# Kernel tuning notes

Measured on AMD Instinct MI355X. Metric: run time of the kernel, lower is better.

Reference implementation:

```python
import jax, jax.numpy as jnp
import numpy as np

LOGISTIC_R = 3.8
COUPLING_ITERS = 5


def _linear_interp(v, L):
    """PyTorch F.interpolate(mode='linear', align_corners=False) along last axis.
    v: [..., K] real -> [..., L] real."""
    K = v.shape[-1]
    pos = (jnp.arange(L, dtype=jnp.float32) + 0.5) * (K / L) - 0.5
    pos = jnp.clip(pos, 0.0, K - 1)  # torch clamps src coords into range
    i0 = jnp.floor(pos).astype(jnp.int32)
    i1 = jnp.minimum(i0 + 1, K - 1)
    w = pos - i0
    return v[..., i0] * (1.0 - w) + v[..., i1] * w


def setup_inputs() -> dict:
    key = jax.random.key(0)
    ks = jax.random.split(key, 4)
    B, Cin, Cout, L, K = 16, 64, 64, 8192, 64
    return {
        "x_real": jax.random.normal(ks[0], (B, Cin, L), jnp.float32),
        "x_imag": jax.random.normal(ks[1], (B, Cin, L), jnp.float32),
        "kernel_real": jax.random.normal(ks[2], (Cout, Cin, K), jnp.float32),
        "kernel_imag": jax.random.normal(ks[3], (Cout, Cin, K), jnp.float32),
        "alpha_D": jnp.ones((1,), jnp.float32),
    }


def reference(x_real, x_imag, kernel_real, kernel_imag, alpha_D):
    x = x_real + 1j * x_imag  # [B, Cin, L] complex64
    L = x.shape[-1]

    # --- logistic self-coupling on magnitude (per-batch min/max over (C, L)) ---
    mag = jnp.abs(x)
    phase = jnp.angle(x)
    mmin = mag.min(axis=(-1, -2), keepdims=True)
    mmax = mag.max(axis=(-1, -2), keepdims=True)
    xn = (mag - mmin) / (mmax - mmin + 1e-10)
    for _ in range(COUPLING_ITERS):
        xn = LOGISTIC_R * xn * (1.0 - xn)
    mag_c = xn * (mmax - mmin) + mmin
    x_coupled = mag_c * jnp.exp(1j * phase)

    # --- spectral conv: FFT, per-pair kernel interpolation, complex MAC ---
    x_fft = jnp.fft.fft(x_coupled, axis=-1)  # [B, Cin, L]
    kfft = jnp.fft.fft(kernel_real + 1j * kernel_imag, axis=-1)  # [O, I, K]
    kmag = _linear_interp(jnp.abs(kfft), L)    # [O, I, L]
    kph = _linear_interp(jnp.angle(kfft), L)   # [O, I, L]
    kint = kmag * jnp.exp(1j * kph)            # [O, I, L] complex64
    out_fft = jnp.einsum('bjl,ijl->bil', x_fft, kint)  # replaces O*I python loop
    out = jnp.fft.ifft(out_fft, axis=-1)  # [B, O, L]

    # --- optical probe activation: sin(omega*0 + phi0 + alpha_D * lambda) ---
    theta = alpha_D[0] * jnp.arange(L, dtype=jnp.float32)
    act = jnp.sin(theta)  # omega*t = 0, phi0 = 0
    return out * act
```

## Files before the change

kernel.cpp:

```cpp
#include <hip/hip_runtime.h>
#include <hip/hip_fp16.h>
#include <hip/hip_bf16.h>
#include <math.h>

#define L 8192
#define LOG2L 13
#define B 16
#define CIN 64
#define COUT 64
#define KK 64

#define PI_F 3.14159265358979323846f

typedef float f4v __attribute__((ext_vector_type(4)));
typedef short s8v __attribute__((ext_vector_type(8)));

__device__ __forceinline__ int swz(int n) { return n ^ ((n >> 8) & 31); }
__device__ __forceinline__ int PHI(int n) { return n ^ ((((n >> 5) ^ (n >> 9)) & 15) << 1); }

__device__ __forceinline__ void nsincos(float ang, float* sn, float* cs) {
    float r = ang * 0.15915494309189535f;
    r = r - floorf(r);
    *sn = __builtin_amdgcn_sinf(r);
    *cs = __builtin_amdgcn_cosf(r);
}

__device__ __forceinline__ unsigned short f2bf(float f) {
    unsigned u = __builtin_bit_cast(unsigned, f);
    u += 0x7FFFu + ((u >> 16) & 1u);
    return (unsigned short)(u >> 16);
}
__device__ __forceinline__ unsigned pkbf(float a, float b) {
    unsigned ua = __builtin_bit_cast(unsigned, a) + 0x8000u;
    unsigned ub = __builtin_bit_cast(unsigned, b) + 0x8000u;
    return (ub & 0xFFFF0000u) | (ua >> 16);
}

template<int INV>
__device__ __forceinline__ void bfly4(float& u0r, float& u0i, float& u1r, float& u1i,
                                      float& v0r, float& v0i, float& v1r, float& v1i,
                                      float w1r, float w1i, float w2r, float w2i) {
    float A0r = u0r + v0r, A0i = u0i + v0i;
    float t0r = u0r - v0r, t0i = u0i - v0i;
    float B0r = t0r * w1r - t0i * w1i, B0i = t0r * w1i + t0i * w1r;
    float A1r = u1r + v1r, A1i = u1i + v1i;
    float t1r = u1r - v1r, t1i = u1i - v1i;
    float wr = t1r * w1r - t1i * w1i, wi = t1r * w1i + t1i * w1r;
    float B1r = INV ? -wi : wi;
    float B1i = INV ? wr : -wr;
    u0r = A0r + A1r; u0i = A0i + A1i;
    float d0r = A0r - A1r, d0i = A0i - A1i;
    u1r = d0r * w2r - d0i * w2i; u1i = d0r * w2i + d0i * w2r;
    v0r = B0r + B1r; v0i = B0i + B1i;
    float d1r = B0r - B1r, d1i = B0i - B1i;
    v1r = d1r * w2r - d1i * w2i; v1i = d1r * w2i + d1i * w2r;
}

template<int INV>
__device__ __forceinline__ void radix16(float* xr, float* xi, float wc, float ws) {
    const float C8 = 0.9238795325112867f, S8 = 0.3826834323650898f, C4 = 0.7071067811865476f;
    float e1r = C8, e1i = INV ? S8 : -S8;
    float e2r = C4, e2i = INV ? C4 : -C4;
    float e3r = S8, e3i = INV ? C8 : -C8;
    float a1r[4], a1i[4], a2r[4], a2i[4];
    a1r[0] = wc;                    a1i[0] = ws;
    a1r[1] = wc * e1r - ws * e1i;   a1i[1] = wc * e1i + ws * e1r;
    a1r[2] = wc * e2r - ws * e2i;   a1i[2] = wc * e2i + ws * e2r;
    a1r[3] = wc * e3r - ws * e3i;   a1i[3] = wc * e3i + ws * e3r;
#pragma unroll
    for (int q = 0; q < 4; ++q) {
        a2r[q] = a1r[q] * a1r[q] - a1i[q] * a1i[q];
        a2i[q] = 2.f * a1r[q] * a1i[q];
    }
    float b1r = a2r[0] * a2r[0] - a2i[0] * a2i[0], b1i = 2.f * a2r[0] * a2i[0];
    float b2r = b1r * b1r - b1i * b1i, b2i = 2.f * b1r * b1i;
#pragma unroll
    for (int q = 0; q < 4; ++q)
        bfly4<INV>(xr[q], xi[q], xr[q + 4], xi[q + 4], xr[q + 8], xi[q + 8],
                   xr[q + 12], xi[q + 12], a1r[q], a1i[q], a2r[q], a2i[q]);
#pragma unroll
    for (int c = 0; c < 4; ++c)
        bfly4<INV>(xr[4 * c], xi[4 * c], xr[4 * c + 1], xi[4 * c + 1],
                   xr[4 * c + 2], xi[4 * c + 2], xr[4 * c + 3], xi[4 * c + 3],
                   b1r, b1i, b2r, b2i);
}

__global__ __launch_bounds__(256) void k_reduce1(const float* __restrict__ xr,
                                                 const float* __restrict__ xi,
                                                 float* __restrict__ pmin,
                                                 float* __restrict__ pmax) {
    int bid = blockIdx.x;
    int batch = bid >> 6, slice = bid & 63;
    size_t base = (size_t)batch * CIN * L + (size_t)slice * L;
    int tid = threadIdx.x;
    float mn = 3.4e38f, mx = 0.0f;
    for (int r = 0; r < 32; ++r) {
        int idx = r * 256 + tid;
        float a = xr[base + idx], b = xi[base + idx];
        float m = sqrtf(a * a + b * b);
        mn = fminf(mn, m);
        mx = fmaxf(mx, m);
    }
    __shared__ float smn[4], smx[4];
    for (int off = 32; off >= 1; off >>= 1) {
        mn = fminf(mn, __shfl_down(mn, off));
        mx = fmaxf(mx, __shfl_down(mx, off));
    }
    int wave = tid >> 6;
    if ((tid & 63) == 0) { smn[wave] = mn; smx[wave] = mx; }
    __syncthreads();
    if (tid == 0) {
        for (int w = 1; w < 4; ++w) { mn = fminf(mn, smn[w]); mx = fmaxf(mx, smx[w]); }
        pmin[bid] = mn;
        pmax[bid] = mx;
    }
}

__global__ __launch_bounds__(64) void k_reduce2(const float* __restrict__ pmin,
                                                const float* __restrict__ pmax,
                                                float* __restrict__ mmin,
                                                float* __restrict__ mmax) {
    int b = blockIdx.x, t = threadIdx.x;
    float mn = pmin[b * 64 + t], mx = pmax[b * 64 + t];
    for (int off = 32; off >= 1; off >>= 1) {
        mn = fminf(mn, __shfl_down(mn, off));
        mx = fmaxf(mx, __shfl_down(mx, off));
    }
    if (t == 0) { mmin[b] = mn; mmax[b] = mx; }
}

__global__ __launch_bounds__(64) void k_kstats(const float* __restrict__ kr,
                                               const float* __restrict__ ki,
                                               float* __restrict__ Pmag,
                                               float* __restrict__ Pph) {
    int row = blockIdx.x;
    int k = threadIdx.x;
    __shared__ float sr[64], si[64];
    sr[k] = kr[row * 64 + k];
    si[k] = ki[row * 64 + k];
    __syncthreads();
    float ar = 0.f, ai = 0.f;
    for (int n = 0; n < 64; ++n) {
        int m = (n * k) & 63;
        float ang = -2.0f * PI_F * (float)m * (1.0f / 64.0f);
        float s, c;
        __sincosf(ang, &s, &c);
        ar += sr[n] * c - si[n] * s;
        ai += sr[n] * s + si[n] * c;
    }
    float mag = sqrtf(ar * ar + ai * ai);
    float ph = atan2f(ai, ar);
    int io = row >> 6, jn = row & 63;
    int ic = io >> 4, l15 = io & 15;
    int jc = jn >> 5, hi = (jn >> 3) & 3, e = jn & 7;
    int lane = hi * 16 + l15;
    size_t off = (size_t)k * 4096 + (ic * 2 + jc) * 512 + lane * 8 + e;
    Pmag[off] = mag;
    Pph[off] = ph;
    if (k == 63) {
        Pmag[off + 4096] = mag;
        Pph[off + 4096] = ph;
    }
}

__global__ __launch_bounds__(512) void k_fwd(const float* __restrict__ xr,
                                             const float* __restrict__ xi,
                                             const float* __restrict__ mmin_,
                                             const float* __restrict__ mmax_,
                                             unsigned* __restrict__ xRd) {
    __shared__ float sRe[L];
    __shared__ float sIm[L];
    int row = blockIdx.x;
    int b = row >> 6;
    int tid = threadIdx.x;
    float mmin = mmin_[b], mmax = mmax_[b];
    float span = mmax - mmin;
    float invden = 1.0f / (span + 1e-10f);
    size_t base = (size_t)row * L;

    float vr[16], vi[16];
#pragma unroll
    for (int r = 0; r < 16; ++r) {
        int idx = r * 512 + tid;
        float a = xr[base + idx], c = xi[base + idx];
        float m = sqrtf(a * a + c * c);
        float xn = (m - mmin) * invden;
#pragma unroll
        for (int it = 0; it < 5; ++it) xn = 3.8f * xn * (1.0f - xn);
        float mc = xn * span + mmin;
        float scale = (m > 0.0f) ? (mc / m) : 0.0f;
        vr[r] = a * scale;
        vi[r] = c * scale;
    }
#pragma unroll
    for (int r = 0; r < 8; ++r) {
        float sn, cs;
        nsincos(-PI_F * (float)(r * 512 + tid) * (1.0f / 4096.0f), &sn, &cs);
        float ar = vr[r], ai = vi[r], br = vr[r + 8], bi = vi[r + 8];
        vr[r] = ar + br; vi[r] = ai + bi;
        float dr = ar - br, di = ai - bi;
        vr[r + 8] = dr * cs - di * sn;
        vi[r + 8] = dr * sn + di * cs;
    }
#pragma unroll
    for (int r = 0; r < 16; ++r) {
        int a = PHI(r * 512 + tid);
        sRe[a] = vr[r]; sIm[a] = vi[r];
    }
    __syncthreads();

    {
        int j1 = tid & 255, bA = (tid >> 8) << 12;
#pragma unroll
        for (int m = 0; m < 16; ++m) {
            int a = PHI(bA + j1 + (m << 8));
            vr[m] = sRe[a]; vi[m] = sIm[a];
        }
        float sn, cs;
        nsincos(-PI_F * (float)j1 * (1.0f / 2048.0f), &sn, &cs);
        radix16<0>(vr, vi, cs, sn);
#pragma unroll
        for (int m = 0; m < 16; ++m) {
            int a = PHI(bA + j1 + (m << 8));
            sRe[a] = vr[m]; sIm[a] = vi[m];
        }
    }
    __syncthreads();
    {
        int j1 = tid & 15, bB = (tid >> 4) << 8;
#pragma unroll
        for (int m = 0; m < 16; ++m) {
            int a = PHI(bB + j1 + (m << 4));
            vr[m] = sRe[a]; vi[m] = sIm[a];
        }
        float sn, cs;
        nsincos(-PI_F * (float)j1 * (1.0f / 128.0f), &sn, &cs);
        radix16<0>(vr, vi, cs, sn);
#pragma unroll
        for (int m = 0; m < 16; ++m) {
            int a = PHI(bB + j1 + (m << 4));
            sRe[a] = vr[m]; sIm[a] = vi[m];
        }
    }
    __syncthreads();
    {
        float2* f2R = (float2*)sRe;
        float2* f2I = (float2*)sIm;
#pragma unroll
        for (int m = 0; m < 8; ++m) {
            int a = PHI(tid * 16 + 2 * m) >> 1;
            float2 vR = f2R[a], vI = f2I[a];
            vr[2 * m] = vR.x; vr[2 * m + 1] = vR.y;
            vi[2 * m] = vI.x; vi[2 * m + 1] = vI.y;
        }
        radix16<0>(vr, vi, 1.0f, 0.0f);
#pragma unroll
        for (int m = 0; m < 8; ++m) {
            int a = PHI(tid * 16 + 2 * m) >> 1;
            f2R[a] = make_float2(vr[2 * m], vr[2 * m + 1]);
            f2I[a] = make_float2(vi[2 * m], vi[2 * m + 1]);
        }
    }
    __syncthreads();

#pragma unroll
    for (int r = 0; r < 16; ++r) {
        int a = PHI(r * 512 + tid);
        vr[r] = sRe[a]; vi[r] = sIm[a];
    }
    __syncthreads();
#pragma unroll
    for (int r = 0; r < 16; ++r) {
        int idx = r * 512 + tid;
        int n = (int)(__brev((unsigned)idx) >> 19);
        int a = swz(n);
        sRe[a] = vr[r]; sIm[a] = vi[r];
    }
    __syncthreads();

    unsigned* xId = xRd + (size_t)1024 * 4096;
#pragma unroll
    for (int r = 0; r < 8; ++r) {
        int n2 = r * 1024 + tid * 2;
        int a0 = swz(n2), a1 = swz(n2 + 1);
        unsigned vR = ((unsigned)f2bf(sRe[a1]) << 16) | f2bf(sRe[a0]);
        unsigned vI = ((unsigned)f2bf(sIm[a1]) << 16) | f2bf(sIm[a0]);
        size_t o = (size_t)row * 4096 + (n2 >> 1);
        xRd[o] = vR;
        xId[o] = vI;
    }
}

#define PB 8
#define REG 4624
__global__ __launch_bounds__(256) void k_gemm(const unsigned short* __restrict__ xp,
                                              const float* __restrict__ Pmag,
                                              const float* __restrict__ Pph,
                                              unsigned* __restrict__ outd) {
    __shared__ uint4 ldsbuf[(PB * REG) / 16];
    char* lds = (char*)ldsbuf;
    int tid = threadIdx.x;
    int bid = blockIdx.x;
    int pwin = ((bid & 7) << 7) + (bid >> 3);
    int p0 = pwin * PB;

#pragma unroll
    for (int r = 0; r < 8; ++r) {
        int u = r * 256 + tid;
        int plane = u >> 10;
        int row = u & 1023;
        uint4 v = *(const uint4*)&xp[(size_t)plane * 8388608 + (size_t)row * 8192 + p0];
        int base = plane * 2304 + (row >> 6) * 144 + (row & 63) * 2;
        unsigned short h[8] = {
            (unsigned short)(v.x & 0xFFFF), (unsigned short)(v.x >> 16),
            (unsigned short)(v.y & 0xFFFF), (unsigned short)(v.y >> 16),
            (unsigned short)(v.z & 0xFFFF), (unsigned short)(v.z >> 16),
            (unsigned short)(v.w & 0xFFFF), (unsigned short)(v.w >> 16)};
#pragma unroll
        for (int e = 0; e < 8; ++e)
            *(unsigned short*)&lds[e * REG + base] = h[e];
    }
    __syncthreads();

    int lane = tid & 63;
    int wid = tid >> 6;
    int l15 = lane & 15, l4 = lane >> 4;

    int pA = p0 + wid * 2;
    float posA = ((float)pA + 0.5f) * (1.0f / 128.0f) - 0.5f;
    posA = fmaxf(posA, 0.0f);
    int i0k = (int)posA;
    bool clamp = (i0k >= KK - 1);
    float wq[2];
#pragma unroll
    for (int q = 0; q < 2; ++q) {
        float pos = ((float)(pA + q) + 0.5f) * (1.0f / 128.0f) - 0.5f;
        pos = fmaxf(pos, 0.0f);
        wq[q] = clamp ? 0.0f : (pos - (float)i0k);
    }
    const float* mb0 = Pmag + (size_t)i0k * 4096;
    const float* pb0 = Pph + (size_t)i0k * 4096;

    f4v accR[2][4], accI[2][4];
#pragma unroll
    for (int q = 0; q < 2; ++q)
#pragma unroll
        for (int ic = 0; ic < 4; ++ic) { accR[q][ic] = (f4v)0.0f; accI[q][ic] = (f4v)0.0f; }

#pragma unroll
    for (int jc = 0; jc < 2; ++jc) {
        int jb2 = (jc * 32 + l4 * 8) * 2;
        s8v xR0 = *(const s8v*)&lds[(wid * 2 + 0) * REG + l15 * 144 + jb2];
        s8v xI0 = *(const s8v*)&lds[(wid * 2 + 0) * REG + 2304 + l15 * 144 + jb2];
        s8v xR1 = *(const s8v*)&lds[(wid * 2 + 1) * REG + l15 * 144 + jb2];
        s8v xI1 = *(const s8v*)&lds[(wid * 2 + 1) * REG + 2304 + l15 * 144 + jb2];
#pragma unroll
        for (int ic = 0; ic < 4; ++ic) {
            int tb = (ic * 2 + jc) * 512 + lane * 8;
            float4 m0a = *(const float4*)(mb0 + tb);
            float4 m0b = *(const float4*)(mb0 + tb + 4);
            float4 m1a = *(const float4*)(mb0 + 4096 + tb);
            float4 m1b = *(const float4*)(mb0 + 4096 + tb + 4);
            float4 q0a = *(const float4*)(pb0 + tb);
            float4 q0b = *(const float4*)(pb0 + tb + 4);
            float4 q1a = *(const float4*)(pb0 + 4096 + tb);
            float4 q1b = *(const float4*)(pb0 + 4096 + tb + 4);
            float m0v[8] = {m0a.x, m0a.y, m0a.z, m0a.w, m0b.x, m0b.y, m0b.z, m0b.w};
            float m1v[8] = {m1a.x, m1a.y, m1a.z, m1a.w, m1b.x, m1b.y, m1b.z, m1b.w};
            float q0v[8] = {q0a.x, q0a.y, q0a.z, q0a.w, q0b.x, q0b.y, q0b.z, q0b.w};
            float q1v[8] = {q1a.x, q1a.y, q1a.z, q1a.w, q1b.x, q1b.y, q1b.z, q1b.w};
#pragma unroll
            for (int q = 0; q < 2; ++q) {
                float w = wq[q];
                float kr[8], ki[8];
#pragma unroll
                for (int e = 0; e < 8; ++e) {
                    float mm = m0v[e] + (m1v[e] - m0v[e]) * w;
                    float ph = q0v[e] + (q1v[e] - q0v[e]) * w;
                    float sn, cs;
                    nsincos(ph, &sn, &cs);
                    kr[e] = mm * cs;
                    ki[e] = mm * sn;
                }
                union { unsigned u[4]; s8v v; } kR, kIp, kIn;
#pragma unroll
                for (int t = 0; t < 4; ++t) {
                    kR.u[t] = pkbf(kr[2 * t], kr[2 * t + 1]);
                    kIp.u[t] = pkbf(ki[2 * t], ki[2 * t + 1]);
                    kIn.u[t] = kIp.u[t] ^ 0x80008000u;
                }
                s8v xR = q ? xR1 : xR0;
                s8v xI = q ? xI1 : xI0;
                accR[q][ic] = __builtin_amdgcn_mfma_f32_16x16x32_bf16(xR, kR.v, accR[q][ic], 0, 0, 0);
                accR[q][ic] = __builtin_amdgcn_mfma_f32_16x16x32_bf16(xI, kIn.v, accR[q][ic], 0, 0, 0);
                accI[q][ic] = __builtin_amdgcn_mfma_f32_16x16x32_bf16(xR, kIp.v, accI[q][ic], 0, 0, 0);
                accI[q][ic] = __builtin_amdgcn_mfma_f32_16x16x32_bf16(xI, kR.v, accI[q][ic], 0, 0, 0);
            }
        }
    }

#pragma unroll
    for (int q = 0; q < 2; ++q) {
        int pp = wid * 2 + q;
#pragma unroll
        for (int ic = 0; ic < 4; ++ic) {
#pragma unroll
            for (int e = 0; e < 4; ++e) {
                int row = (l4 * 4 + e) * 64 + ic * 16 + l15;
                unsigned val = ((unsigned)f2bf(accI[q][ic][e]) << 16) | f2bf(accR[q][ic][e]);
                *(unsigned*)&lds[pp * REG + row * 4] = val;
            }
        }
    }
    __syncthreads();

#pragma unroll
    for (int k = 0; k < 32; ++k) {
        int row = k * 32 + (tid >> 3);
        unsigned v = *(const unsigned*)&lds[(tid & 7) * REG + row * 4];
        outd[(size_t)row * 8192 + p0 + (tid & 7)] = v;
    }
}

__global__ __launch_bounds__(512) void k_ifft(const __hip_bfloat162* __restrict__ outfft,
                                              const float* __restrict__ alpha_,
                                              float* __restrict__ out) {
    __shared__ float sRe[L];
    __shared__ float sIm[L];
    int row = blockIdx.x;
    int tid = threadIdx.x;
    float alpha = alpha_[0];
    size_t base = (size_t)row * L;

    float vr[16], vi[16];
#pragma unroll
    for (int r = 0; r < 16; ++r) {
        __hip_bfloat162 v = outfft[base + r * 512 + tid];
        vr[r] = __bfloat162float(v.x);
        vi[r] = __bfloat162float(v.y);
    }
#pragma unroll
    for (int r = 0; r < 8; ++r) {
        float sn, cs;
        nsincos(PI_F * (float)(r * 512 + tid) * (1.0f / 4096.0f), &sn, &cs);
        float ar = vr[r], ai = vi[r], br = vr[r + 8], bi = vi[r + 8];
        vr[r] = ar + br; vi[r] = ai + bi;
        float dr = ar - br, di = ai - bi;
        vr[r + 8] = dr * cs - di * sn;
        vi[r + 8] = dr * sn + di * cs;
    }
#pragma unroll
    for (int r = 0; r < 16; ++r) {
        int a = PHI(r * 512 + tid);
        sRe[a] = vr[r]; sIm[a] = vi[r];
    }
    __syncthreads();

    {
        int j1 = tid & 255, bA = (tid >> 8) << 12;
#pragma unroll
        for (int m = 0; m < 16; ++m) {
            int a = PHI(bA + j1 + (m << 8));
            vr[m] = sRe[a]; vi[m] = sIm[a];
        }
        float sn, cs;
        nsincos(PI_F * (float)j1 * (1.0f / 2048.0f), &sn, &cs);
        radix16<1>(vr, vi, cs, sn);
#pragma unroll
        for (int m = 0; m < 16; ++m) {
            int a = PHI(bA + j1 + (m << 8));
            sRe[a] = vr[m]; sIm[a] = vi[m];
        }
    }
    __syncthreads();
    {
        int j1 = tid & 15, bB = (tid >> 4) << 8;
#pragma unroll
        for (int m = 0; m < 16; ++m) {
            int a = PHI(bB + j1 + (m << 4));
            vr[m] = sRe[a]; vi[m] = sIm[a];
        }
        float sn, cs;
        nsincos(PI_F * (float)j1 * (1.0f / 128.0f), &sn, &cs);
        radix16<1>(vr, vi, cs, sn);
#pragma unroll
        for (int m = 0; m < 16; ++m) {
            int a = PHI(bB + j1 + (m << 4));
            sRe[a] = vr[m]; sIm[a] = vi[m];
        }
    }
    __syncthreads();
    {
        float2* f2R = (float2*)sRe;
        float2* f2I = (float2*)sIm;
#pragma unroll
        for (int m = 0; m < 8; ++m) {
            int a = PHI(tid * 16 + 2 * m) >> 1;
            float2 vR = f2R[a], vI = f2I[a];
            vr[2 * m] = vR.x; vr[2 * m + 1] = vR.y;
            vi[2 * m] = vI.x; vi[2 * m + 1] = vI.y;
        }
        radix16<1>(vr, vi, 1.0f, 0.0f);
#pragma unroll
        for (int m = 0; m < 8; ++m) {
            int a = PHI(tid * 16 + 2 * m) >> 1;
            f2R[a] = make_float2(vr[2 * m], vr[2 * m + 1]);
            f2I[a] = make_float2(vi[2 * m], vi[2 * m + 1]);
        }
    }
    __syncthreads();

#pragma unroll
    for (int r = 0; r < 16; ++r) {
        int a = PHI(r * 512 + tid);
        vr[r] = sRe[a]; vi[r] = sIm[a];
    }
    __syncthreads();
#pragma unroll
    for (int r = 0; r < 16; ++r) {
        int idx = r * 512 + tid;
        int n = (int)(__brev((unsigned)idx) >> 19);
        int a = swz(n);
        sRe[a] = vr[r]; sIm[a] = vi[r];
    }
    __syncthreads();

    const float invN = 1.0f / (float)L;
#pragma unroll
    for (int rpt = 0; rpt < L / 512; ++rpt) {
        int n = rpt * 512 + tid;
        float act = sinf(alpha * (float)n);
        out[base + n] = sRe[swz(n)] * act * invN;
    }
}

extern "C" void kernel_launch(void* const* d_in, const int* in_sizes, int n_in,
                              void* d_out, int out_size, void* d_ws, size_t ws_size,
                              hipStream_t stream) {
    const float* xr = (const float*)d_in[0];
    const float* xi = (const float*)d_in[1];
    const float* kr = (const float*)d_in[2];
    const float* ki = (const float*)d_in[3];
    const float* alpha = (const float*)d_in[4];
    float* out = (float*)d_out;

    char* ws = (char*)d_ws;
    size_t OFFT_BYTES = (size_t)B * COUT * L * 4;
    size_t TBL_BYTES = (size_t)65 * 4096 * 4;
    unsigned* outfft_d = (unsigned*)ws;
    float* Pmag = (float*)(ws + OFFT_BYTES);
    float* Pph  = (float*)(ws + OFFT_BYTES + TBL_BYTES);
    float* pmin = (float*)(ws + OFFT_BYTES + 2 * TBL_BYTES);
    float* pmax = pmin + 1024;
    float* mmin = pmax + 1024;
    float* mmax = mmin + 16;

    unsigned* xplanar = (unsigned*)d_out;

    hipLaunchKernelGGL(k_reduce1, dim3(1024), dim3(256), 0, stream, xr, xi, pmin, pmax);
    hipLaunchKernelGGL(k_reduce2, dim3(16), dim3(64), 0, stream, pmin, pmax, mmin, mmax);
    hipLaunchKernelGGL(k_kstats, dim3(4096), dim3(64), 0, stream, kr, ki, Pmag, Pph);
    hipLaunchKernelGGL(k_fwd, dim3(1024), dim3(512), 0, stream, xr, xi, mmin, mmax, xplanar);
    hipLaunchKernelGGL(k_gemm, dim3(1024), dim3(256), 0, stream,
                       (const unsigned short*)xplanar, Pmag, Pph, outfft_d);
    hipLaunchKernelGGL(k_ifft, dim3(1024), dim3(512), 0, stream,
                       (const __hip_bfloat162*)outfft_d, alpha, out);
}
```

Measured before the change: 135.9 us.

## Write FFT output frequency-major interleaved and widen GEMM block to 16 frequencies

The forward FFT kernel now writes interleaved bf16 real/imag pairs in a frequency-tile-major layout, so each GEMM block reads one contiguous 64KB chunk instead of strided 16-byte pieces from two planar arrays. The GEMM kernel handles 16 frequencies per block with 512 threads, uses a padded LDS row stride, unpacks real/imag per lane, and writes its output with 64-byte vector stores. The aim is coalesced global traffic in the GEMM staging and writeback. In exchange, the FFT kernel's stores become more scattered, and LDS use and register pressure per block go up.

Result: slower. 209.4 us (+54.0%).

```diff
diff --git a/kernel.cpp b/kernel.cpp
--- a/kernel.cpp
+++ b/kernel.cpp
@@ -167,7 +167,7 @@
                                              const float* __restrict__ xi,
                                              const float* __restrict__ mmin_,
                                              const float* __restrict__ mmax_,
-                                             unsigned* __restrict__ xRd) {
+                                             unsigned* __restrict__ Xd) {
     __shared__ float sRe[L];
     __shared__ float sIm[L];
     int row = blockIdx.x;
@@ -278,100 +278,102 @@
     }
     __syncthreads();
 
-    unsigned* xId = xRd + (size_t)1024 * 4096;
-#pragma unroll
-    for (int r = 0; r < 8; ++r) {
-        int n2 = r * 1024 + tid * 2;
-        int a0 = swz(n2), a1 = swz(n2 + 1);
-        unsigned vR = ((unsigned)f2bf(sRe[a1]) << 16) | f2bf(sRe[a0]);
-        unsigned vI = ((unsigned)f2bf(sIm[a1]) << 16) | f2bf(sIm[a0]);
-        size_t o = (size_t)row * 4096 + (n2 >> 1);
-        xRd[o] = vR;
-        xId[o] = vI;
-    }
-}
-
-#define PB 8
-#define REG 4624
-__global__ __launch_bounds__(256) void k_gemm(const unsigned short* __restrict__ xp,
+    {
+        unsigned o16[16];
+        int mask = (tid >> 4) & 31;
+#pragma unroll
+        for (int pi = 0; pi < 16; ++pi) {
+            int a = (tid * 16 + pi) ^ mask;
+            o16[pi] = ((unsigned)f2bf(sIm[a]) << 16) | f2bf(sRe[a]);
+        }
+        size_t ob = (size_t)tid * 16384 + (size_t)row * 16;
+#pragma unroll
+        for (int k = 0; k < 4; ++k)
+            *(uint4*)&Xd[ob + 4 * k] = make_uint4(o16[4 * k], o16[4 * k + 1],
+                                                  o16[4 * k + 2], o16[4 * k + 3]);
+    }
+}
+
+#define PBG 16
+#define RSTR 1092
+__global__ __launch_bounds__(512) void k_gemm(const unsigned* __restrict__ X,
                                               const float* __restrict__ Pmag,
                                               const float* __restrict__ Pph,
                                               unsigned* __restrict__ outd) {
-    __shared__ uint4 ldsbuf[(PB * REG) / 16];
-    char* lds = (char*)ldsbuf;
+    __shared__ unsigned lds[PBG * RSTR];
     int tid = threadIdx.x;
     int bid = blockIdx.x;
-    int pwin = ((bid & 7) << 7) + (bid >> 3);
-    int p0 = pwin * PB;
-
-#pragma unroll
-    for (int r = 0; r < 8; ++r) {
-        int u = r * 256 + tid;
-        int plane = u >> 10;
-        int row = u & 1023;
-        uint4 v = *(const uint4*)&xp[(size_t)plane * 8388608 + (size_t)row * 8192 + p0];
-        int base = plane * 2304 + (row >> 6) * 144 + (row & 63) * 2;
-        unsigned short h[8] = {
-            (unsigned short)(v.x & 0xFFFF), (unsigned short)(v.x >> 16),
-            (unsigned short)(v.y & 0xFFFF), (unsigned short)(v.y >> 16),
-            (unsigned short)(v.z & 0xFFFF), (unsigned short)(v.z >> 16),
-            (unsigned short)(v.w & 0xFFFF), (unsigned short)(v.w >> 16)};
-#pragma unroll
-        for (int e = 0; e < 8; ++e)
-            *(unsigned short*)&lds[e * REG + base] = h[e];
-    }
-    __syncthreads();
-
-    int lane = tid & 63;
-    int wid = tid >> 6;
+    int pwin = ((bid & 7) << 6) + (bid >> 3);
+    int p0 = pwin * PBG;
+    const unsigned* src = X + (size_t)pwin * 16384;
+
+#pragma unroll
+    for (int k = 0; k < 8; ++k) {
+        int u = k * 512 + tid;
+        uint4 v = *(const uint4*)&src[(size_t)u * 4];
+        int row = u >> 2;
+        int pi0 = (u & 3) * 4;
+        int gr = row + ((row >> 6) << 2);
+        lds[(pi0 + 0) * RSTR + gr] = v.x;
+        lds[(pi0 + 1) * RSTR + gr] = v.y;
+        lds[(pi0 + 2) * RSTR + gr] = v.z;
+        lds[(pi0 + 3) * RSTR + gr] = v.w;
+    }
+    __syncthreads();
+
+    int lane = tid & 63, wid = tid >> 6;
     int l15 = lane & 15, l4 = lane >> 4;
 
     int pA = p0 + wid * 2;
     float posA = ((float)pA + 0.5f) * (1.0f / 128.0f) - 0.5f;
     posA = fmaxf(posA, 0.0f);
     int i0k = (int)posA;
-    bool clamp = (i0k >= KK - 1);
+    bool clampv = (i0k >= KK - 1);
     float wq[2];
 #pragma unroll
     for (int q = 0; q < 2; ++q) {
         float pos = ((float)(pA + q) + 0.5f) * (1.0f / 128.0f) - 0.5f;
         pos = fmaxf(pos, 0.0f);
-        wq[q] = clamp ? 0.0f : (pos - (float)i0k);
+        wq[q] = clampv ? 0.0f : (pos - (float)i0k);
     }
     const float* mb0 = Pmag + (size_t)i0k * 4096;
     const float* pb0 = Pph + (size_t)i0k * 4096;
 
-    f4v accR[2][4], accI[2][4];
-#pragma unroll
-    for (int q = 0; q < 2; ++q)
-#pragma unroll
-        for (int ic = 0; ic < 4; ++ic) { accR[q][ic] = (f4v)0.0f; accI[q][ic] = (f4v)0.0f; }
-
-#pragma unroll
-    for (int jc = 0; jc < 2; ++jc) {
-        int jb2 = (jc * 32 + l4 * 8) * 2;
-        s8v xR0 = *(const s8v*)&lds[(wid * 2 + 0) * REG + l15 * 144 + jb2];
-        s8v xI0 = *(const s8v*)&lds[(wid * 2 + 0) * REG + 2304 + l15 * 144 + jb2];
-        s8v xR1 = *(const s8v*)&lds[(wid * 2 + 1) * REG + l15 * 144 + jb2];
-        s8v xI1 = *(const s8v*)&lds[(wid * 2 + 1) * REG + 2304 + l15 * 144 + jb2];
-#pragma unroll
-        for (int ic = 0; ic < 4; ++ic) {
-            int tb = (ic * 2 + jc) * 512 + lane * 8;
-            float4 m0a = *(const float4*)(mb0 + tb);
-            float4 m0b = *(const float4*)(mb0 + tb + 4);
-            float4 m1a = *(const float4*)(mb0 + 4096 + tb);
-            float4 m1b = *(const float4*)(mb0 + 4096 + tb + 4);
-            float4 q0a = *(const float4*)(pb0 + tb);
-            float4 q0b = *(const float4*)(pb0 + tb + 4);
-            float4 q1a = *(const float4*)(pb0 + 4096 + tb);
-            float4 q1b = *(const float4*)(pb0 + 4096 + tb + 4);
-            float m0v[8] = {m0a.x, m0a.y, m0a.z, m0a.w, m0b.x, m0b.y, m0b.z, m0b.w};
-            float m1v[8] = {m1a.x, m1a.y, m1a.z, m1a.w, m1b.x, m1b.y, m1b.z, m1b.w};
-            float q0v[8] = {q0a.x, q0a.y, q0a.z, q0a.w, q0b.x, q0b.y, q0b.z, q0b.w};
-            float q1v[8] = {q1a.x, q1a.y, q1a.z, q1a.w, q1b.x, q1b.y, q1b.z, q1b.w};
-#pragma unroll
-            for (int q = 0; q < 2; ++q) {
-                float w = wq[q];
+#pragma unroll
+    for (int q = 0; q < 2; ++q) {
+        int pp = wid * 2 + q;
+        float w = wq[q];
+        f4v aR[4], aI[4];
+#pragma unroll
+        for (int ic = 0; ic < 4; ++ic) { aR[ic] = (f4v)0.0f; aI[ic] = (f4v)0.0f; }
+
+#pragma unroll
+        for (int jc = 0; jc < 2; ++jc) {
+            int rb = pp * RSTR + l15 * 68 + jc * 32 + l4 * 8;
+            uint4 d0 = *(const uint4*)&lds[rb];
+            uint4 d1 = *(const uint4*)&lds[rb + 4];
+            unsigned dwv[8] = {d0.x, d0.y, d0.z, d0.w, d1.x, d1.y, d1.z, d1.w};
+            union { unsigned u[4]; s8v v; } xR, xI;
+#pragma unroll
+            for (int kk = 0; kk < 4; ++kk) {
+                xR.u[kk] = (dwv[2 * kk] & 0xFFFFu) | (dwv[2 * kk + 1] << 16);
+                xI.u[kk] = (dwv[2 * kk] >> 16) | (dwv[2 * kk + 1] & 0xFFFF0000u);
+            }
+#pragma unroll
+            for (int ic = 0; ic < 4; ++ic) {
+                int tb = (ic * 2 + jc) * 512 + lane * 8;
+                float4 m0a = *(const float4*)(mb0 + tb);
+                float4 m0b = *(const float4*)(mb0 + tb + 4);
+                float4 m1a = *(const float4*)(mb0 + 4096 + tb);
+                float4 m1b = *(const float4*)(mb0 + 4096 + tb + 4);
+                float4 q0a = *(const float4*)(pb0 + tb);
+                float4 q0b = *(const float4*)(pb0 + tb + 4);
+                float4 q1a = *(const float4*)(pb0 + 4096 + tb);
+                float4 q1b = *(const float4*)(pb0 + 4096 + tb + 4);
+                float m0v[8] = {m0a.x, m0a.y, m0a.z, m0a.w, m0b.x, m0b.y, m0b.z, m0b.w};
+                float m1v[8] = {m1a.x, m1a.y, m1a.z, m1a.w, m1b.x, m1b.y, m1b.z, m1b.w};
+                float q0v[8] = {q0a.x, q0a.y, q0a.z, q0a.w, q0b.x, q0b.y, q0b.z, q0b.w};
+                float q1v[8] = {q1a.x, q1a.y, q1a.z, q1a.w, q1b.x, q1b.y, q1b.z, q1b.w};
                 float kr[8], ki[8];
 #pragma unroll
                 for (int e = 0; e < 8; ++e) {
@@ -389,36 +391,37 @@
                     kIp.u[t] = pkbf(ki[2 * t], ki[2 * t + 1]);
                     kIn.u[t] = kIp.u[t] ^ 0x80008000u;
                 }
-                s8v xR = q ? xR1 : xR0;
-                s8v xI = q ? xI1 : xI0;
-                accR[q][ic] = __builtin_amdgcn_mfma_f32_16x16x32_bf16(xR, kR.v, accR[q][ic], 0, 0, 0);
-                accR[q][ic] = __builtin_amdgcn_mfma_f32_16x16x32_bf16(xI, kIn.v, accR[q][ic], 0, 0, 0);
-                accI[q][ic] = __builtin_amdgcn_mfma_f32_16x16x32_bf16(xR, kIp.v, accI[q][ic], 0, 0, 0);
-                accI[q][ic] = __builtin_amdgcn_mfma_f32_16x16x32_bf16(xI, kR.v, accI[q][ic], 0, 0, 0);
+                aR[ic] = __builtin_amdgcn_mfma_f32_16x16x32_bf16(xR.v, kR.v, aR[ic], 0, 0, 0);
+                aR[ic] = __builtin_amdgcn_mfma_f32_16x16x32_bf16(xI.v, kIn.v, aR[ic], 0, 0, 0);
+                aI[ic] = __builtin_amdgcn_mfma_f32_16x16x32_bf16(xR.v, kIp.v, aI[ic], 0, 0, 0);
+                aI[ic] = __builtin_amdgcn_mfma_f32_16x16x32_bf16(xI.v, kR.v, aI[ic], 0, 0, 0);
             }
         }
-    }
-
-#pragma unroll
-    for (int q = 0; q < 2; ++q) {
-        int pp = wid * 2 + q;
-#pragma unroll
-        for (int ic = 0; ic < 4; ++ic) {
+
+#pragma unroll
+        for (int ic = 0; ic < 4; ++ic)
 #pragma unroll
             for (int e = 0; e < 4; ++e) {
-                int row = (l4 * 4 + e) * 64 + ic * 16 + l15;
-                unsigned val = ((unsigned)f2bf(accI[q][ic][e]) << 16) | f2bf(accR[q][ic][e]);
-                *(unsigned*)&lds[pp * REG + row * 4] = val;
+                int ro = (l4 * 4 + e) * 64 + ic * 16 + l15;
+                int gro = ro + ((ro >> 6) << 2);
+                lds[pp * RSTR + gro] =
+                    ((unsigned)f2bf(aI[ic][e]) << 16) | f2bf(aR[ic][e]);
             }
-        }
-    }
-    __syncthreads();
-
-#pragma unroll
-    for (int k = 0; k < 32; ++k) {
-        int row = k * 32 + (tid >> 3);
-        unsigned v = *(const unsigned*)&lds[(tid & 7) * REG + row * 4];
-        outd[(size_t)row * 8192 + p0 + (tid & 7)] = v;
+    }
+    __syncthreads();
+
+#pragma unroll
+    for (int rr = 0; rr < 2; ++rr) {
+        int row = rr * 512 + tid;
+        int gr = row + ((row >> 6) << 2);
+        unsigned o[16];
+#pragma unroll
+        for (int pi = 0; pi < 16; ++pi) o[pi] = lds[pi * RSTR + gr];
+        size_t ob = (size_t)row * 8192 + p0;
+#pragma unroll
+        for (int k = 0; k < 4; ++k)
+            *(uint4*)&outd[ob + 4 * k] = make_uint4(o[4 * k], o[4 * k + 1],
+                                                    o[4 * k + 2], o[4 * k + 3]);
     }
 }
 
@@ -555,14 +558,13 @@
     float* mmin = pmax + 1024;
     float* mmax = mmin + 16;
 
-    unsigned* xplanar = (unsigned*)d_out;
+    unsigned* Xd = (unsigned*)d_out;
 
     hipLaunchKernelGGL(k_reduce1, dim3(1024), dim3(256), 0, stream, xr, xi, pmin, pmax);
     hipLaunchKernelGGL(k_reduce2, dim3(16), dim3(64), 0, stream, pmin, pmax, mmin, mmax);
     hipLaunchKernelGGL(k_kstats, dim3(4096), dim3(64), 0, stream, kr, ki, Pmag, Pph);
-    hipLaunchKernelGGL(k_fwd, dim3(1024), dim3(512), 0, stream, xr, xi, mmin, mmax, xplanar);
-    hipLaunchKernelGGL(k_gemm, dim3(1024), dim3(256), 0, stream,
-                       (const unsigned short*)xplanar, Pmag, Pph, outfft_d);
+    hipLaunchKernelGGL(k_fwd, dim3(1024), dim3(512), 0, stream, xr, xi, mmin, mmax, Xd);
+    hipLaunchKernelGGL(k_gemm, dim3(512), dim3(512), 0, stream, Xd, Pmag, Pph, outfft_d);
     hipLaunchKernelGGL(k_ifft, dim3(1024), dim3(512), 0, stream,
                        (const __hip_bfloat162*)outfft_d, alpha, out);
 }
```
